# Optimization experiments

Hardware: AMD Instinct MI355X
Metric: run time of the kernel (lower is better)

Reference implementation:

```python
import jax, jax.numpy as jnp
import numpy as np

T, N, E, F_IN, H_GNN, H_OUT, RH, G, C = 8, 10000, 160000, 128, 128, 128, 128, 32, 10


def gcn_layer(x, src, dst, W, b):
    # PyG GCNConv: h = D^-1/2 (A+I) D^-1/2 (x W) + b, self-loops added, edge weight 1
    h = x @ W  # [N, H]
    ones = jnp.ones((E,), h.dtype)
    deg = jax.ops.segment_sum(ones, dst, num_segments=N) + 1.0  # +1 for self-loop
    dinv = jax.lax.rsqrt(deg)
    coef = dinv[src] * dinv[dst]  # [E]
    agg = jax.ops.segment_sum(h[src] * coef[:, None], dst, num_segments=N)
    agg = agg + h * (dinv * dinv)[:, None]  # self-loop term
    return agg + b


def snapshot_encode(x, edge_index, batch, W1, b1, W2, b2):
    src, dst = edge_index[0], edge_index[1]
    h = jax.nn.relu(gcn_layer(x, src, dst, W1, b1))
    h = jax.nn.relu(gcn_layer(h, src, dst, W2, b2))
    sums = jax.ops.segment_sum(h, batch, num_segments=G)  # global_mean_pool
    cnts = jax.ops.segment_sum(jnp.ones((N,), h.dtype), batch, num_segments=G)
    return sums / jnp.maximum(cnts, 1.0)[:, None]  # [G, H_OUT]


def gru_layer(seq, Wih, Whh, bih, bhh):
    # seq: [T, G, in]; torch nn.GRU cell equations
    H = Whh.shape[1]

    def step(h, xt):
        gi = xt @ Wih.T + bih
        gh = h @ Whh.T + bhh
        ir, iz, inn = jnp.split(gi, 3, axis=-1)
        hr, hz, hn = jnp.split(gh, 3, axis=-1)
        r = jax.nn.sigmoid(ir + hr)
        z = jax.nn.sigmoid(iz + hz)
        n = jnp.tanh(inn + r * hn)
        h_new = (1.0 - z) * n + z * h
        return h_new, h_new

    h0 = jnp.zeros((seq.shape[1], H), seq.dtype)
    hT, outs = jax.lax.scan(step, h0, seq)
    return outs, hT


def setup_inputs() -> dict:
    key = jax.random.key(0)
    ks = jax.random.split(key, 20)
    s = 0.05
    inp = {
        "x": jax.random.normal(ks[0], (T, N, F_IN), jnp.float32),
        "edge_index": jax.random.randint(ks[1], (T, 2, E), 0, N),
        "batch": jax.random.randint(ks[2], (T, N), 0, G),
        "W1": jax.random.normal(ks[3], (F_IN, H_GNN), jnp.float32) * s,
        "b1": jnp.zeros((H_GNN,), jnp.float32),
        "W2": jax.random.normal(ks[4], (H_GNN, H_OUT), jnp.float32) * s,
        "b2": jnp.zeros((H_OUT,), jnp.float32),
        "Wih0": jax.random.normal(ks[5], (3 * RH, H_OUT), jnp.float32) * s,
        "Whh0": jax.random.normal(ks[6], (3 * RH, RH), jnp.float32) * s,
        "bih0": jnp.zeros((3 * RH,), jnp.float32),
        "bhh0": jnp.zeros((3 * RH,), jnp.float32),
        "Wih1": jax.random.normal(ks[7], (3 * RH, RH), jnp.float32) * s,
        "Whh1": jax.random.normal(ks[8], (3 * RH, RH), jnp.float32) * s,
        "bih1": jnp.zeros((3 * RH,), jnp.float32),
        "bhh1": jnp.zeros((3 * RH,), jnp.float32),
        "Wc": jax.random.normal(ks[9], (C, RH), jnp.float32) * s,
        "bc": jnp.zeros((C,), jnp.float32),
    }
    return inp


def reference(x, edge_index, batch, W1, b1, W2, b2, Wih0, Whh0, bih0, bhh0,
              Wih1, Whh1, bih1, bhh1, Wc, bc):
    # per-snapshot GNN encode, vmapped over T snapshots -> [T, G, H_OUT]
    emb = jax.vmap(snapshot_encode, in_axes=(0, 0, 0, None, None, None, None))(
        x, edge_index, batch, W1, b1, W2, b2)
    outs, _ = gru_layer(emb, Wih0, Whh0, bih0, bhh0)
    _, hT = gru_layer(outs, Wih1, Whh1, bih1, bhh1)  # h_n[-1]: last layer final state
    return hT @ Wc.T + bc  # [G, C]
```

## Files before the change

### kernel.cpp

```cpp
#include <hip/hip_runtime.h>

#define T_ 8
#define N_ 10000
#define E_ 160000
#define G_ 32
#define C_ 10
#define F_ 128

typedef _Float16 f16;
typedef _Float16 f16x2 __attribute__((ext_vector_type(2)));
typedef _Float16 f16x4 __attribute__((ext_vector_type(4)));
typedef _Float16 f16x8 __attribute__((ext_vector_type(8)));
typedef float floatx4 __attribute__((ext_vector_type(4)));

static constexpr size_t ROWS = (size_t)T_ * N_;
static constexpr int SLICE = E_ / 8;

static constexpr size_t OFF_XH    = 0;
static constexpr size_t OFF_A1    = 20480000;
static constexpr size_t OFF_H1    = 40960000;
static constexpr size_t OFF_REC   = 61440000;
static constexpr size_t OFF_CNT   = 66560000;
static constexpr size_t OFF_DINV  = 69120000;
static constexpr size_t OFF_RP    = 69440000;
static constexpr size_t OFF_CNTG  = 69760032;
static constexpr size_t OFF_BRP   = 69761056;
static constexpr size_t OFF_WP    = 69762112;
static constexpr size_t OFF_BLIST = 69827648;
static constexpr size_t OFF_EMBH  = 70147648;
static constexpr size_t OFF_GPACK = 70213184;
static constexpr size_t OFF_GI0   = 70606400;
static constexpr size_t OFF_PART  = 70999616;

__device__ __forceinline__ float sig_fast(float x) {
  return __builtin_amdgcn_rcpf(1.0f + __builtin_amdgcn_exp2f(-1.4426950408889634f * x));
}
__device__ __forceinline__ float tanh_fast(float x) {
  return 1.0f - 2.0f * __builtin_amdgcn_rcpf(1.0f + __builtin_amdgcn_exp2f(2.8853900817779268f * x));
}

__global__ __launch_bounds__(1024) void hist_kernel(const int* __restrict__ ei,
                                                    const int* __restrict__ batch,
                                                    int* __restrict__ cnt,
                                                    int* __restrict__ cntG) {
  __shared__ int hL[N_];
  __shared__ int cL[G_];
  int b = blockIdx.x, tid = threadIdx.x;
  int t = b & 7, s = b >> 3;
  for (int i = tid; i < N_; i += 1024) hL[i] = 0;
  if (tid < G_) cL[tid] = 0;
  __syncthreads();
  const int* dstp = ei + (size_t)t * 2 * E_ + E_ + s * SLICE;
  for (int e4 = tid; e4 < SLICE / 4; e4 += 1024) {
    int4 d = *(const int4*)(dstp + e4 * 4);
    atomicAdd(&hL[d.x], 1); atomicAdd(&hL[d.y], 1);
    atomicAdd(&hL[d.z], 1); atomicAdd(&hL[d.w], 1);
  }
  if (s == 0)
    for (int n = tid; n < N_; n += 1024) atomicAdd(&cL[batch[t * N_ + n]], 1);
  __syncthreads();
  int* cp = cnt + ((size_t)t * 8 + s) * N_;
  for (int i = tid; i < N_; i += 1024) cp[i] = hL[i];
  if (s == 0 && tid < G_) cntG[t * G_ + tid] = cL[tid];
}

__global__ __launch_bounds__(1024) void scan_kernel(int* __restrict__ cnt,
                                                    int* __restrict__ rp,
                                                    float* __restrict__ dinv,
                                                    const int* __restrict__ cntG,
                                                    int* __restrict__ brp) {
  __shared__ int wsum[16];
  __shared__ int carry;
  int t = blockIdx.x, tid = threadIdx.x, lane = tid & 63, wid = tid >> 6;
  if (t == 8) {
    int v = (tid < 256) ? cntG[tid] : 0;
    for (int ofs = 1; ofs < 64; ofs <<= 1) {
      int u = __shfl_up(v, ofs);
      if (lane >= ofs) v += u;
    }
    if (lane == 63 && wid < 4) wsum[wid] = v;
    __syncthreads();
    if (tid < 256) {
      int base = 0;
      for (int w = 0; w < wid; ++w) base += wsum[w];
      if (tid == 0) brp[0] = 0;
      brp[tid + 1] = v + base;
    }
    return;
  }
  if (tid == 0) { carry = 0; rp[t * (N_ + 1)] = 0; }
  __syncthreads();
  for (int c0 = 0; c0 < N_; c0 += 1024) {
    int n = c0 + tid;
    int vs[8];
    int deg = 0;
    if (n < N_) {
#pragma unroll
      for (int s = 0; s < 8; ++s) {
        vs[s] = cnt[((size_t)t * 8 + s) * N_ + n];
        deg += vs[s];
      }
      dinv[t * N_ + n] = rsqrtf((float)deg + 1.0f);
    }
    int v = (n < N_) ? deg : 0;
    int v0 = v;
    for (int ofs = 1; ofs < 64; ofs <<= 1) {
      int u = __shfl_up(v, ofs);
      if (lane >= ofs) v += u;
    }
    if (lane == 63) wsum[wid] = v;
    __syncthreads();
    if (wid == 0) {
      int w = (lane < 16) ? wsum[lane] : 0;
      for (int ofs = 1; ofs < 16; ofs <<= 1) {
        int u = __shfl_up(w, ofs);
        if (lane >= ofs) w += u;
      }
      if (lane < 16) wsum[lane] = w;
    }
    __syncthreads();
    int base = carry + (wid ? wsum[wid - 1] : 0);
    if (n < N_) {
      rp[t * (N_ + 1) + n + 1] = base + v;
      int run = base + v - v0;
#pragma unroll
      for (int s = 0; s < 8; ++s) {
        int vv = vs[s];
        cnt[((size_t)t * 8 + s) * N_ + n] = run;
        run += vv;
      }
    }
    __syncthreads();
    if (tid == 0) carry += wsum[15];
    __syncthreads();
  }
}

__global__ __launch_bounds__(1024) void fill_kernel(const int* __restrict__ ei,
                                                    const int* __restrict__ base,
                                                    int* __restrict__ rec,
                                                    const int* __restrict__ batch,
                                                    const int* __restrict__ brp,
                                                    int* __restrict__ blist) {
  __shared__ int offL[N_];
  __shared__ int cb[G_];
  int b = blockIdx.x, tid = threadIdx.x;
  int t = b & 7, s = b >> 3;
  const int* bp = base + ((size_t)t * 8 + s) * N_;
  for (int i = tid; i < N_; i += 1024) offL[i] = bp[i];
  if (s == 0 && tid < G_) cb[tid] = brp[t * G_ + tid];
  __syncthreads();
  const int* srcp = ei + (size_t)t * 2 * E_ + s * SLICE;
  const int* dstp = srcp + E_;
  int* rt = rec + (size_t)t * E_;
  for (int e4 = tid; e4 < SLICE / 4; e4 += 1024) {
    int4 sv = *(const int4*)(srcp + e4 * 4);
    int4 dv = *(const int4*)(dstp + e4 * 4);
    int p0 = atomicAdd(&offL[dv.x], 1);
    int p1 = atomicAdd(&offL[dv.y], 1);
    int p2 = atomicAdd(&offL[dv.z], 1);
    int p3 = atomicAdd(&offL[dv.w], 1);
    rt[p0] = sv.x; rt[p1] = sv.y; rt[p2] = sv.z; rt[p3] = sv.w;
  }
  if (s == 0) {
    for (int n = tid; n < N_; n += 1024) {
      int g = batch[t * N_ + n];
      int p = atomicAdd(&cb[g], 1);
      blist[p] = t * N_ + n;
    }
  }
}

__global__ void cvt_kernel(const float* __restrict__ x, const float* __restrict__ dinv,
                           f16* __restrict__ xh) {
  size_t i = ((size_t)blockIdx.x * 256 + threadIdx.x) * 4;
  float4 v = *(const float4*)(x + i);
  float d = dinv[i >> 7];
  f16x4 o; o.x = (f16)(v.x * d); o.y = (f16)(v.y * d);
  o.z = (f16)(v.z * d); o.w = (f16)(v.w * d);
  *(f16x4*)(xh + i) = o;
}

__global__ void agg_kernel(const f16* __restrict__ X, f16* __restrict__ A,
                           const int* __restrict__ rp, const int* __restrict__ rec,
                           const float* __restrict__ dinv) {
  int wave = threadIdx.x >> 6, lane = threadIdx.x & 63;
  int b = blockIdx.x;
  int t = b & 7, i = b >> 3;
  int n = i * 4 + wave;
  int row = t * N_ + n;
  float ds = dinv[row];
  f16x2 xv = *(const f16x2*)(X + (size_t)row * F_ + 2 * lane);
  float a00 = (float)xv.x, a01 = (float)xv.y;
  float a10 = 0.f, a11 = 0.f, a20 = 0.f, a21 = 0.f, a30 = 0.f, a31 = 0.f;
  int beg = rp[t * (N_ + 1) + n], end = rp[t * (N_ + 1) + n + 1];
  beg = __builtin_amdgcn_readfirstlane(beg);
  end = __builtin_amdgcn_readfirstlane(end);
  const int* rc = rec + (size_t)t * E_;
  const f16* Xt = X + (size_t)t * N_ * F_;
  int e = beg;
  int i0 = 0, i1 = 0, i2 = 0, i3 = 0;
  if (e + 3 < end) { i0 = rc[e]; i1 = rc[e + 1]; i2 = rc[e + 2]; i3 = rc[e + 3]; }
  for (; e + 7 < end; e += 4) {
    int n0 = rc[e + 4], n1 = rc[e + 5], n2 = rc[e + 6], n3 = rc[e + 7];
    f16x2 h0 = *(const f16x2*)(Xt + (size_t)i0 * F_ + 2 * lane);
    f16x2 h1 = *(const f16x2*)(Xt + (size_t)i1 * F_ + 2 * lane);
    f16x2 h2 = *(const f16x2*)(Xt + (size_t)i2 * F_ + 2 * lane);
    f16x2 h3 = *(const f16x2*)(Xt + (size_t)i3 * F_ + 2 * lane);
    a00 += (float)h0.x; a01 += (float)h0.y;
    a10 += (float)h1.x; a11 += (float)h1.y;
    a20 += (float)h2.x; a21 += (float)h2.y;
    a30 += (float)h3.x; a31 += (float)h3.y;
    i0 = n0; i1 = n1; i2 = n2; i3 = n3;
  }
  if (e + 3 < end) {
    f16x2 h0 = *(const f16x2*)(Xt + (size_t)i0 * F_ + 2 * lane);
    f16x2 h1 = *(const f16x2*)(Xt + (size_t)i1 * F_ + 2 * lane);
    f16x2 h2 = *(const f16x2*)(Xt + (size_t)i2 * F_ + 2 * lane);
    f16x2 h3 = *(const f16x2*)(Xt + (size_t)i3 * F_ + 2 * lane);
    a00 += (float)h0.x; a01 += (float)h0.y;
    a10 += (float)h1.x; a11 += (float)h1.y;
    a20 += (float)h2.x; a21 += (float)h2.y;
    a30 += (float)h3.x; a31 += (float)h3.y;
    e += 4;
  }
  for (; e < end; ++e) {
    int s = rc[e];
    f16x2 hv = *(const f16x2*)(Xt + (size_t)s * F_ + 2 * lane);
    a00 += (float)hv.x; a01 += (float)hv.y;
  }
  float r0 = ds * ((a00 + a10) + (a20 + a30));
  float r1 = ds * ((a01 + a11) + (a21 + a31));
  f16x2 o; o.x = (f16)r0; o.y = (f16)r1;
  *(f16x2*)(A + (size_t)row * F_ + 2 * lane) = o;
}

__global__ void packall_kernel(const float* __restrict__ W1, const float* __restrict__ W2,
                               f16* __restrict__ Wp,
                               const float* __restrict__ A0, const float* __restrict__ A1,
                               const float* __restrict__ A2, const float* __restrict__ A3,
                               f16* __restrict__ gp) {
  int idx = blockIdx.x * 256 + threadIdx.x;
  if (idx < 32768) {
    const float* W = (idx < 16384) ? W1 : W2;
    int l = idx & 16383;
    int j = l & 7, lane = (l >> 3) & 63, ct = (l >> 9) & 7, kc = (l >> 12) & 3;
    int k = kc * 32 + ((lane >> 4) & 3) * 8 + j;
    int n = ct * 16 + (lane & 15);
    Wp[idx] = (f16)W[k * 128 + n];
  } else {
    int gidx = idx - 32768;
    int mat = gidx / 49152, l = gidx - mat * 49152;
    int j = l & 7, lane = (l >> 3) & 63, kc = (l >> 9) & 3, nt = l >> 11;
    int k = kc * 32 + ((lane >> 4) & 3) * 8 + j;
    int u = nt * 16 + (lane & 15);
    const float* W = (mat == 0) ? A0 : (mat == 1) ? A1 : (mat == 2) ? A2 : A3;
    gp[gidx] = (f16)W[u * 128 + k];
  }
}

__global__ __launch_bounds__(256) void gemm_kernel(const f16* __restrict__ A,
                                                   const f16* __restrict__ Wp,
                                                   const float* __restrict__ bias,
                                                   const float* __restrict__ scale,
                                                   f16* __restrict__ O) {
  __shared__ f16x8 Bp[2048];
  const f16x8* Wv = (const f16x8*)Wp;
  for (int i = threadIdx.x; i < 2048; i += 256) Bp[i] = Wv[i];
  __syncthreads();
  int wave = threadIdx.x >> 6, lane = threadIdx.x & 63;
  int quad = lane >> 4, m = lane & 15;
  int rowbase = blockIdx.x * 64 + wave * 16;
  const f16x8* Arow = (const f16x8*)(A + (size_t)(rowbase + m) * F_);
  floatx4 acc[8];
#pragma unroll
  for (int ct = 0; ct < 8; ++ct) { floatx4 z = {0.f, 0.f, 0.f, 0.f}; acc[ct] = z; }
#pragma unroll
  for (int kc = 0; kc < 4; ++kc) {
    f16x8 a = Arow[kc * 4 + quad];
#pragma unroll
    for (int ct = 0; ct < 8; ++ct)
      acc[ct] = __builtin_amdgcn_mfma_f32_16x16x32_f16(a, Bp[(kc * 8 + ct) * 64 + lane],
                                                       acc[ct], 0, 0, 0);
  }
  float sv[4];
#pragma unroll
  for (int r = 0; r < 4; ++r)
    sv[r] = scale ? scale[rowbase + quad * 4 + r] : 1.0f;
#pragma unroll
  for (int ct = 0; ct < 8; ++ct) {
    int colc = ct * 16 + m;
    float bv = bias[colc];
#pragma unroll
    for (int r = 0; r < 4; ++r) {
      int row = rowbase + quad * 4 + r;
      float v = fmaxf(acc[ct][r] + bv, 0.0f) * sv[r];
      O[(size_t)row * F_ + colc] = (f16)v;
    }
  }
}

__global__ void pool1_kernel(const f16* __restrict__ H, const int* __restrict__ brp,
                             const int* __restrict__ blist, float* __restrict__ part) {
  int b = blockIdx.x;
  int wave = threadIdx.x >> 6, lane = threadIdx.x & 63;
  int idx = b >> 1;
  int s = (b & 1) * 4 + wave;
  int beg = brp[idx], end = brp[idx + 1];
  beg = __builtin_amdgcn_readfirstlane(beg);
  end = __builtin_amdgcn_readfirstlane(end);
  int len = end - beg;
  int lo = beg + (int)(((long long)len * s) >> 3);
  int hi = beg + (int)(((long long)len * (s + 1)) >> 3);
  float a00 = 0.f, a01 = 0.f, a10 = 0.f, a11 = 0.f;
  float a20 = 0.f, a21 = 0.f, a30 = 0.f, a31 = 0.f;
  int e = lo;
  for (; e + 3 < hi; e += 4) {
    int r0 = blist[e], r1 = blist[e + 1], r2 = blist[e + 2], r3 = blist[e + 3];
    f16x2 v0 = *(const f16x2*)(H + (size_t)r0 * F_ + 2 * lane);
    f16x2 v1 = *(const f16x2*)(H + (size_t)r1 * F_ + 2 * lane);
    f16x2 v2 = *(const f16x2*)(H + (size_t)r2 * F_ + 2 * lane);
    f16x2 v3 = *(const f16x2*)(H + (size_t)r3 * F_ + 2 * lane);
    a00 += (float)v0.x; a01 += (float)v0.y;
    a10 += (float)v1.x; a11 += (float)v1.y;
    a20 += (float)v2.x; a21 += (float)v2.y;
    a30 += (float)v3.x; a31 += (float)v3.y;
  }
  for (; e < hi; ++e) {
    int r = blist[e];
    f16x2 v = *(const f16x2*)(H + (size_t)r * F_ + 2 * lane);
    a00 += (float)v.x; a01 += (float)v.y;
  }
  float2 o;
  o.x = (a00 + a10) + (a20 + a30);
  o.y = (a01 + a11) + (a21 + a31);
  *(float2*)(part + ((size_t)idx * 8 + s) * F_ + 2 * lane) = o;
}

__global__ void pool2_kernel(const float* __restrict__ part, const int* __restrict__ brp,
                             f16* __restrict__ embh) {
  int idx = blockIdx.x * 2 + (threadIdx.x >> 7);
  int f = threadIdx.x & 127;
  float s = 0.f;
#pragma unroll
  for (int k = 0; k < 8; ++k) s += part[((size_t)idx * 8 + k) * F_ + f];
  int cnt = brp[idx + 1] - brp[idx];
  embh[(size_t)idx * F_ + f] = (f16)(s / fmaxf((float)cnt, 1.0f));
}

__global__ __launch_bounds__(256) void gi0_kernel(const f16* __restrict__ embh,
                                                  const f16* __restrict__ gp,
                                                  float* __restrict__ gi0) {
  int wave = threadIdx.x >> 6, lane = threadIdx.x & 63;
  int quad = lane >> 4, mm = lane & 15;
  int rowbase = blockIdx.x * 64 + wave * 16;
  const f16* Arow = embh + (size_t)(rowbase + mm) * 128;
  floatx4 acc[24];
#pragma unroll
  for (int nt = 0; nt < 24; ++nt) { floatx4 z = {0.f, 0.f, 0.f, 0.f}; acc[nt] = z; }
#pragma unroll
  for (int kc = 0; kc < 4; ++kc) {
    f16x8 a = *(const f16x8*)(Arow + kc * 32 + quad * 8);
#pragma unroll
    for (int nt = 0; nt < 24; ++nt) {
      f16x8 b = *(const f16x8*)(gp + (size_t)(((nt * 4 + kc) * 64 + lane)) * 8);
      acc[nt] = __builtin_amdgcn_mfma_f32_16x16x32_f16(a, b, acc[nt], 0, 0, 0);
    }
  }
#pragma unroll
  for (int nt = 0; nt < 24; ++nt)
#pragma unroll
    for (int r = 0; r < 4; ++r)
      gi0[(size_t)(rowbase + quad * 4 + r) * 384 + nt * 16 + mm] = acc[nt][r];
}

__global__ __launch_bounds__(256, 1) void gru_fused(
    const f16* __restrict__ gp, const float* __restrict__ gi0,
    const float* __restrict__ bih0, const float* __restrict__ bhh0,
    const float* __restrict__ bih1, const float* __restrict__ bhh1,
    const float* __restrict__ Wc, const float* __restrict__ bc,
    float* __restrict__ out) {
  __shared__ f16 hb0[16 * 136];
  __shared__ f16 hb1[16 * 136];
  __shared__ float ghb[2 * 384];
  __shared__ float gib[2 * 384];
  __shared__ float h1s[2 * 128];
  int tid = threadIdx.x, wave = tid >> 6, lane = tid & 63;
  int quad = lane >> 4, mm = lane & 15;
  int g2 = tid >> 7, f = tid & 127;
  int bid = blockIdx.x;

  f16x8 B0[24], B1[24];
#pragma unroll
  for (int i = 0; i < 6; ++i)
#pragma unroll
    for (int kc = 0; kc < 4; ++kc) {
      size_t off = (size_t)((((wave * 6 + i) * 4 + kc) * 64 + lane)) * 8;
      B0[i * 4 + kc] = *(const f16x8*)(gp + 1 * 49152 + off);
      B1[i * 4 + kc] = *(const f16x8*)(gp + 3 * 49152 + off);
    }
  float br0 = bih0[f] + bhh0[f];
  float bz0 = bih0[128 + f] + bhh0[128 + f];
  float bni0 = bih0[256 + f], bnh0 = bhh0[256 + f];
  float br1 = bih1[f] + bhh1[f];
  float bz1 = bih1[128 + f] + bhh1[128 + f];
  float bni1 = bih1[256 + f], bnh1 = bhh1[256 + f];

  for (int i = tid; i < 16 * 136; i += 256) { hb0[i] = (f16)0.f; hb1[i] = (f16)0.f; }
  float h0 = 0.f, h1 = 0.f;
  __syncthreads();

  const f16* wih1 = gp + 2 * 49152;
  for (int t = 0; t < T_; ++t) {
    f16x8 Bs[24];
#pragma unroll
    for (int i = 0; i < 6; ++i)
#pragma unroll
      for (int kc = 0; kc < 4; ++kc)
        Bs[i * 4 + kc] = *(const f16x8*)(wih1 +
            (size_t)((((wave * 6 + i) * 4 + kc) * 64 + lane)) * 8);
    const float* gi = gi0 + (size_t)(t * G_ + bid * 2 + g2) * 384;
    float gir = gi[f], giz = gi[128 + f], gin = gi[256 + f];

    floatx4 acc[6];
#pragma unroll
    for (int i = 0; i < 6; ++i) { floatx4 z = {0.f, 0.f, 0.f, 0.f}; acc[i] = z; }
#pragma unroll
    for (int kc = 0; kc < 4; ++kc) {
      f16x8 a = *(const f16x8*)(hb0 + mm * 136 + kc * 32 + quad * 8);
#pragma unroll
      for (int i = 0; i < 6; ++i)
        acc[i] = __builtin_amdgcn_mfma_f32_16x16x32_f16(a, B0[i * 4 + kc], acc[i], 0, 0, 0);
    }
    if (quad == 0) {
#pragma unroll
      for (int i = 0; i < 6; ++i) {
        ghb[0 * 384 + wave * 96 + i * 16 + mm] = acc[i][0];
        ghb[1 * 384 + wave * 96 + i * 16 + mm] = acc[i][1];
      }
    }
    __syncthreads();

    {
      float hr = ghb[g2 * 384 + f];
      float hz = ghb[g2 * 384 + 128 + f];
      float hn = ghb[g2 * 384 + 256 + f];
      float r = sig_fast(gir + hr + br0);
      float z = sig_fast(giz + hz + bz0);
      float nn = tanh_fast(gin + bni0 + r * (hn + bnh0));
      h0 = (1.0f - z) * nn + z * h0;
      hb0[g2 * 136 + f] = (f16)h0;
    }
    __syncthreads();

    floatx4 accx[6], acch[6];
#pragma unroll
    for (int i = 0; i < 6; ++i) {
      floatx4 z = {0.f, 0.f, 0.f, 0.f}; accx[i] = z; acch[i] = z;
    }
#pragma unroll
    for (int kc = 0; kc < 4; ++kc) {
      f16x8 ax = *(const f16x8*)(hb0 + mm * 136 + kc * 32 + quad * 8);
      f16x8 ah = *(const f16x8*)(hb1 + mm * 136 + kc * 32 + quad * 8);
#pragma unroll
      for (int i = 0; i < 6; ++i) {
        accx[i] = __builtin_amdgcn_mfma_f32_16x16x32_f16(ax, Bs[i * 4 + kc], accx[i], 0, 0, 0);
        acch[i] = __builtin_amdgcn_mfma_f32_16x16x32_f16(ah, B1[i * 4 + kc], acch[i], 0, 0, 0);
      }
    }
    if (quad == 0) {
#pragma unroll
      for (int i = 0; i < 6; ++i) {
        gib[0 * 384 + wave * 96 + i * 16 + mm] = accx[i][0];
        gib[1 * 384 + wave * 96 + i * 16 + mm] = accx[i][1];
        ghb[0 * 384 + wave * 96 + i * 16 + mm] = acch[i][0];
        ghb[1 * 384 + wave * 96 + i * 16 + mm] = acch[i][1];
      }
    }
    __syncthreads();

    {
      float i1r = gib[g2 * 384 + f];
      float i1z = gib[g2 * 384 + 128 + f];
      float i1n = gib[g2 * 384 + 256 + f];
      float hr = ghb[g2 * 384 + f];
      float hz = ghb[g2 * 384 + 128 + f];
      float hn = ghb[g2 * 384 + 256 + f];
      float r = sig_fast(i1r + hr + br1);
      float z = sig_fast(i1z + hz + bz1);
      float nn = tanh_fast(i1n + bni1 + r * (hn + bnh1));
      h1 = (1.0f - z) * nn + z * h1;
      hb1[g2 * 136 + f] = (f16)h1;
    }
    __syncthreads();
  }

  h1s[g2 * 128 + f] = h1;
  __syncthreads();
  if (tid < 2 * C_) {
    int gg = tid / C_, c = tid - gg * C_;
    float s = bc[c];
    const float* wr = Wc + (size_t)c * 128;
    const float* hr = h1s + gg * 128;
    for (int k = 0; k < 128; k += 4) {
      float4 w = *(const float4*)(wr + k);
      s += hr[k] * w.x + hr[k + 1] * w.y + hr[k + 2] * w.z + hr[k + 3] * w.w;
    }
    out[(bid * 2 + gg) * C_ + c] = s;
  }
}

extern "C" void kernel_launch(void* const* d_in, const int* in_sizes, int n_in,
                              void* d_out, int out_size, void* d_ws, size_t ws_size,
                              hipStream_t stream) {
  const float* x    = (const float*)d_in[0];
  const int*   ei   = (const int*)d_in[1];
  const int*   batch= (const int*)d_in[2];
  const float* W1   = (const float*)d_in[3];
  const float* b1   = (const float*)d_in[4];
  const float* W2   = (const float*)d_in[5];
  const float* b2   = (const float*)d_in[6];
  const float* Wih0 = (const float*)d_in[7];
  const float* Whh0 = (const float*)d_in[8];
  const float* bih0 = (const float*)d_in[9];
  const float* bhh0 = (const float*)d_in[10];
  const float* Wih1 = (const float*)d_in[11];
  const float* Whh1 = (const float*)d_in[12];
  const float* bih1 = (const float*)d_in[13];
  const float* bhh1 = (const float*)d_in[14];
  const float* Wc   = (const float*)d_in[15];
  const float* bc   = (const float*)d_in[16];
  float* out = (float*)d_out;

  char* ws = (char*)d_ws;
  f16*   Xh    = (f16*)(ws + OFF_XH);
  f16*   A1    = (f16*)(ws + OFF_A1);
  f16*   H1    = (f16*)(ws + OFF_H1);
  f16*   A2    = A1;
  f16*   H2    = Xh;
  int*   rec   = (int*)(ws + OFF_REC);
  int*   cnt   = (int*)(ws + OFF_CNT);
  float* dinv  = (float*)(ws + OFF_DINV);
  int*   rp    = (int*)(ws + OFF_RP);
  int*   cntG  = (int*)(ws + OFF_CNTG);
  int*   brp   = (int*)(ws + OFF_BRP);
  f16*   Wp    = (f16*)(ws + OFF_WP);
  int*   blist = (int*)(ws + OFF_BLIST);
  f16*   embh  = (f16*)(ws + OFF_EMBH);
  f16*   gp    = (f16*)(ws + OFF_GPACK);
  float* gi0   = (float*)(ws + OFF_GI0);
  float* part  = (float*)(ws + OFF_PART);

  packall_kernel<<<896, 256, 0, stream>>>(W1, W2, Wp, Wih0, Whh0, Wih1, Whh1, gp);
  hist_kernel<<<64, 1024, 0, stream>>>(ei, batch, cnt, cntG);
  scan_kernel<<<9, 1024, 0, stream>>>(cnt, rp, dinv, cntG, brp);
  cvt_kernel<<<10000, 256, 0, stream>>>(x, dinv, Xh);
  fill_kernel<<<64, 1024, 0, stream>>>(ei, cnt, rec, batch, brp, blist);

  agg_kernel<<<20000, 256, 0, stream>>>(Xh, A1, rp, rec, dinv);
  gemm_kernel<<<1250, 256, 0, stream>>>(A1, Wp, b1, dinv, H1);
  agg_kernel<<<20000, 256, 0, stream>>>(H1, A2, rp, rec, dinv);
  gemm_kernel<<<1250, 256, 0, stream>>>(A2, Wp + 16384, b2, (const float*)nullptr, H2);

  pool1_kernel<<<512, 256, 0, stream>>>(H2, brp, blist, part);
  pool2_kernel<<<128, 256, 0, stream>>>(part, brp, embh);
  gi0_kernel<<<4, 256, 0, stream>>>(embh, gp, gi0);
  gru_fused<<<16, 256, 0, stream>>>(gp, gi0, bih0, bhh0, bih1, bhh1, Wc, bc, out);
}
```

Measured before the change: 307.9 us.

## Fuse neighbor aggregation into GEMM and fold pooling/gi0 into GRU kernel

Each GCN layer now runs as one kernel: a block gathers and sums neighbor rows for 64 nodes into shared memory, then multiplies that tile with the weight via MFMA. This removes the intermediate aggregate buffer round-trip and two launches. The final mean-pool reduction and the layer-0 input projection are moved into the GRU kernel's prologue, which removes two more small launches. The cost is less parallelism: 1256 blocks each doing 16 serial gathers per wave instead of 20000 blocks, so latency hiding during the gather may suffer.

Result: slower. 344.0 us (+11.7%).

```diff
diff --git a/kernel.cpp b/kernel.cpp
--- a/kernel.cpp
+++ b/kernel.cpp
@@ -27,9 +27,7 @@
 static constexpr size_t OFF_BRP   = 69761056;
 static constexpr size_t OFF_WP    = 69762112;
 static constexpr size_t OFF_BLIST = 69827648;
-static constexpr size_t OFF_EMBH  = 70147648;
 static constexpr size_t OFF_GPACK = 70213184;
-static constexpr size_t OFF_GI0   = 70606400;
 static constexpr size_t OFF_PART  = 70999616;
 
 __device__ __forceinline__ float sig_fast(float x) {
@@ -179,60 +177,6 @@
   f16x4 o; o.x = (f16)(v.x * d); o.y = (f16)(v.y * d);
   o.z = (f16)(v.z * d); o.w = (f16)(v.w * d);
   *(f16x4*)(xh + i) = o;
-}
-
-__global__ void agg_kernel(const f16* __restrict__ X, f16* __restrict__ A,
-                           const int* __restrict__ rp, const int* __restrict__ rec,
-                           const float* __restrict__ dinv) {
-  int wave = threadIdx.x >> 6, lane = threadIdx.x & 63;
-  int b = blockIdx.x;
-  int t = b & 7, i = b >> 3;
-  int n = i * 4 + wave;
-  int row = t * N_ + n;
-  float ds = dinv[row];
-  f16x2 xv = *(const f16x2*)(X + (size_t)row * F_ + 2 * lane);
-  float a00 = (float)xv.x, a01 = (float)xv.y;
-  float a10 = 0.f, a11 = 0.f, a20 = 0.f, a21 = 0.f, a30 = 0.f, a31 = 0.f;
-  int beg = rp[t * (N_ + 1) + n], end = rp[t * (N_ + 1) + n + 1];
-  beg = __builtin_amdgcn_readfirstlane(beg);
-  end = __builtin_amdgcn_readfirstlane(end);
-  const int* rc = rec + (size_t)t * E_;
-  const f16* Xt = X + (size_t)t * N_ * F_;
-  int e = beg;
-  int i0 = 0, i1 = 0, i2 = 0, i3 = 0;
-  if (e + 3 < end) { i0 = rc[e]; i1 = rc[e + 1]; i2 = rc[e + 2]; i3 = rc[e + 3]; }
-  for (; e + 7 < end; e += 4) {
-    int n0 = rc[e + 4], n1 = rc[e + 5], n2 = rc[e + 6], n3 = rc[e + 7];
-    f16x2 h0 = *(const f16x2*)(Xt + (size_t)i0 * F_ + 2 * lane);
-    f16x2 h1 = *(const f16x2*)(Xt + (size_t)i1 * F_ + 2 * lane);
-    f16x2 h2 = *(const f16x2*)(Xt + (size_t)i2 * F_ + 2 * lane);
-    f16x2 h3 = *(const f16x2*)(Xt + (size_t)i3 * F_ + 2 * lane);
-    a00 += (float)h0.x; a01 += (float)h0.y;
-    a10 += (float)h1.x; a11 += (float)h1.y;
-    a20 += (float)h2.x; a21 += (float)h2.y;
-    a30 += (float)h3.x; a31 += (float)h3.y;
-    i0 = n0; i1 = n1; i2 = n2; i3 = n3;
-  }
-  if (e + 3 < end) {
-    f16x2 h0 = *(const f16x2*)(Xt + (size_t)i0 * F_ + 2 * lane);
-    f16x2 h1 = *(const f16x2*)(Xt + (size_t)i1 * F_ + 2 * lane);
-    f16x2 h2 = *(const f16x2*)(Xt + (size_t)i2 * F_ + 2 * lane);
-    f16x2 h3 = *(const f16x2*)(Xt + (size_t)i3 * F_ + 2 * lane);
-    a00 += (float)h0.x; a01 += (float)h0.y;
-    a10 += (float)h1.x; a11 += (float)h1.y;
-    a20 += (float)h2.x; a21 += (float)h2.y;
-    a30 += (float)h3.x; a31 += (float)h3.y;
-    e += 4;
-  }
-  for (; e < end; ++e) {
-    int s = rc[e];
-    f16x2 hv = *(const f16x2*)(Xt + (size_t)s * F_ + 2 * lane);
-    a00 += (float)hv.x; a01 += (float)hv.y;
-  }
-  float r0 = ds * ((a00 + a10) + (a20 + a30));
-  float r1 = ds * ((a01 + a11) + (a21 + a31));
-  f16x2 o; o.x = (f16)r0; o.y = (f16)r1;
-  *(f16x2*)(A + (size_t)row * F_ + 2 * lane) = o;
 }
 
 __global__ void packall_kernel(const float* __restrict__ W1, const float* __restrict__ W2,
@@ -259,25 +203,90 @@
   }
 }
 
-__global__ __launch_bounds__(256) void gemm_kernel(const f16* __restrict__ A,
-                                                   const f16* __restrict__ Wp,
-                                                   const float* __restrict__ bias,
-                                                   const float* __restrict__ scale,
-                                                   f16* __restrict__ O) {
+template <int SCALE>
+__global__ __launch_bounds__(256) void agg_gemm_kernel(
+    const f16* __restrict__ X, const f16* __restrict__ Wp,
+    const float* __restrict__ bias, const float* __restrict__ dinv,
+    const int* __restrict__ rp, const int* __restrict__ rec,
+    f16* __restrict__ O) {
   __shared__ f16x8 Bp[2048];
+  __shared__ f16 At[64][136];
+  int tid = threadIdx.x;
   const f16x8* Wv = (const f16x8*)Wp;
-  for (int i = threadIdx.x; i < 2048; i += 256) Bp[i] = Wv[i];
-  __syncthreads();
-  int wave = threadIdx.x >> 6, lane = threadIdx.x & 63;
-  int quad = lane >> 4, m = lane & 15;
-  int rowbase = blockIdx.x * 64 + wave * 16;
-  const f16x8* Arow = (const f16x8*)(A + (size_t)(rowbase + m) * F_);
+  for (int i = tid; i < 2048; i += 256) Bp[i] = Wv[i];
+  __syncthreads();
+
+  int wave = tid >> 6, lane = tid & 63;
+  int b = blockIdx.x;
+  int t = b & 7, chunk = b >> 3;
+  int nbase = chunk * 64 + wave * 16;
+
+  const int* rpt = rp + t * (N_ + 1);
+  int rpv = 0;
+  if (lane <= 16 && nbase + lane <= N_) rpv = rpt[nbase + lane];
+  float dv = 0.f;
+  if (lane < 16 && nbase + lane < N_) dv = dinv[t * N_ + nbase + lane];
+
+  const f16* Xt = X + (size_t)t * N_ * F_;
+  const int* rc = rec + (size_t)t * E_;
+
+  for (int rr = 0; rr < 16; ++rr) {
+    int n = nbase + rr;
+    f16x2 o;
+    if (n < N_) {
+      int beg = __builtin_amdgcn_readfirstlane(__shfl(rpv, rr));
+      int end = __builtin_amdgcn_readfirstlane(__shfl(rpv, rr + 1));
+      float ds = __shfl(dv, rr);
+      f16x2 xv = *(const f16x2*)(Xt + (size_t)n * F_ + 2 * lane);
+      float a00 = (float)xv.x, a01 = (float)xv.y;
+      float a10 = 0.f, a11 = 0.f, a20 = 0.f, a21 = 0.f, a30 = 0.f, a31 = 0.f;
+      int e = beg;
+      int i0 = 0, i1 = 0, i2 = 0, i3 = 0;
+      if (e + 3 < end) { i0 = rc[e]; i1 = rc[e + 1]; i2 = rc[e + 2]; i3 = rc[e + 3]; }
+      for (; e + 7 < end; e += 4) {
+        int n0 = rc[e + 4], n1 = rc[e + 5], n2 = rc[e + 6], n3 = rc[e + 7];
+        f16x2 h0 = *(const f16x2*)(Xt + (size_t)i0 * F_ + 2 * lane);
+        f16x2 h1 = *(const f16x2*)(Xt + (size_t)i1 * F_ + 2 * lane);
+        f16x2 h2 = *(const f16x2*)(Xt + (size_t)i2 * F_ + 2 * lane);
+        f16x2 h3 = *(const f16x2*)(Xt + (size_t)i3 * F_ + 2 * lane);
+        a00 += (float)h0.x; a01 += (float)h0.y;
+        a10 += (float)h1.x; a11 += (float)h1.y;
+        a20 += (float)h2.x; a21 += (float)h2.y;
+        a30 += (float)h3.x; a31 += (float)h3.y;
+        i0 = n0; i1 = n1; i2 = n2; i3 = n3;
+      }
+      if (e + 3 < end) {
+        f16x2 h0 = *(const f16x2*)(Xt + (size_t)i0 * F_ + 2 * lane);
+        f16x2 h1 = *(const f16x2*)(Xt + (size_t)i1 * F_ + 2 * lane);
+        f16x2 h2 = *(const f16x2*)(Xt + (size_t)i2 * F_ + 2 * lane);
+        f16x2 h3 = *(const f16x2*)(Xt + (size_t)i3 * F_ + 2 * lane);
+        a00 += (float)h0.x; a01 += (float)h0.y;
+        a10 += (float)h1.x; a11 += (float)h1.y;
+        a20 += (float)h2.x; a21 += (float)h2.y;
+        a30 += (float)h3.x; a31 += (float)h3.y;
+        e += 4;
+      }
+      for (; e < end; ++e) {
+        int s = rc[e];
+        f16x2 hv = *(const f16x2*)(Xt + (size_t)s * F_ + 2 * lane);
+        a00 += (float)hv.x; a01 += (float)hv.y;
+      }
+      float r0 = ds * ((a00 + a10) + (a20 + a30));
+      float r1 = ds * ((a01 + a11) + (a21 + a31));
+      o.x = (f16)r0; o.y = (f16)r1;
+    } else {
+      o.x = (f16)0.f; o.y = (f16)0.f;
+    }
+    *(f16x2*)(&At[wave * 16 + rr][2 * lane]) = o;
+  }
+
+  int quad = lane >> 4, mm = lane & 15;
   floatx4 acc[8];
 #pragma unroll
   for (int ct = 0; ct < 8; ++ct) { floatx4 z = {0.f, 0.f, 0.f, 0.f}; acc[ct] = z; }
 #pragma unroll
   for (int kc = 0; kc < 4; ++kc) {
-    f16x8 a = Arow[kc * 4 + quad];
+    f16x8 a = *(const f16x8*)(&At[wave * 16 + mm][kc * 32 + quad * 8]);
 #pragma unroll
     for (int ct = 0; ct < 8; ++ct)
       acc[ct] = __builtin_amdgcn_mfma_f32_16x16x32_f16(a, Bp[(kc * 8 + ct) * 64 + lane],
@@ -286,16 +295,18 @@
   float sv[4];
 #pragma unroll
   for (int r = 0; r < 4; ++r)
-    sv[r] = scale ? scale[rowbase + quad * 4 + r] : 1.0f;
+    sv[r] = SCALE ? __shfl(dv, quad * 4 + r) : 1.0f;
 #pragma unroll
   for (int ct = 0; ct < 8; ++ct) {
-    int colc = ct * 16 + m;
+    int colc = ct * 16 + mm;
     float bv = bias[colc];
 #pragma unroll
     for (int r = 0; r < 4; ++r) {
-      int row = rowbase + quad * 4 + r;
-      float v = fmaxf(acc[ct][r] + bv, 0.0f) * sv[r];
-      O[(size_t)row * F_ + colc] = (f16)v;
+      int n = nbase + quad * 4 + r;
+      if (n < N_) {
+        float v = fmaxf(acc[ct][r] + bv, 0.0f) * sv[r];
+        O[((size_t)t * N_ + n) * F_ + colc] = (f16)v;
+      }
     }
   }
 }
@@ -337,49 +348,15 @@
   *(float2*)(part + ((size_t)idx * 8 + s) * F_ + 2 * lane) = o;
 }
 
-__global__ void pool2_kernel(const float* __restrict__ part, const int* __restrict__ brp,
-                             f16* __restrict__ embh) {
-  int idx = blockIdx.x * 2 + (threadIdx.x >> 7);
-  int f = threadIdx.x & 127;
-  float s = 0.f;
-#pragma unroll
-  for (int k = 0; k < 8; ++k) s += part[((size_t)idx * 8 + k) * F_ + f];
-  int cnt = brp[idx + 1] - brp[idx];
-  embh[(size_t)idx * F_ + f] = (f16)(s / fmaxf((float)cnt, 1.0f));
-}
-
-__global__ __launch_bounds__(256) void gi0_kernel(const f16* __restrict__ embh,
-                                                  const f16* __restrict__ gp,
-                                                  float* __restrict__ gi0) {
-  int wave = threadIdx.x >> 6, lane = threadIdx.x & 63;
-  int quad = lane >> 4, mm = lane & 15;
-  int rowbase = blockIdx.x * 64 + wave * 16;
-  const f16* Arow = embh + (size_t)(rowbase + mm) * 128;
-  floatx4 acc[24];
-#pragma unroll
-  for (int nt = 0; nt < 24; ++nt) { floatx4 z = {0.f, 0.f, 0.f, 0.f}; acc[nt] = z; }
-#pragma unroll
-  for (int kc = 0; kc < 4; ++kc) {
-    f16x8 a = *(const f16x8*)(Arow + kc * 32 + quad * 8);
-#pragma unroll
-    for (int nt = 0; nt < 24; ++nt) {
-      f16x8 b = *(const f16x8*)(gp + (size_t)(((nt * 4 + kc) * 64 + lane)) * 8);
-      acc[nt] = __builtin_amdgcn_mfma_f32_16x16x32_f16(a, b, acc[nt], 0, 0, 0);
-    }
-  }
-#pragma unroll
-  for (int nt = 0; nt < 24; ++nt)
-#pragma unroll
-    for (int r = 0; r < 4; ++r)
-      gi0[(size_t)(rowbase + quad * 4 + r) * 384 + nt * 16 + mm] = acc[nt][r];
-}
-
-__global__ __launch_bounds__(256, 1) void gru_fused(
-    const f16* __restrict__ gp, const float* __restrict__ gi0,
+__global__ __launch_bounds__(256, 1) void gru_mega(
+    const f16* __restrict__ gp, const float* __restrict__ part,
+    const int* __restrict__ brp,
     const float* __restrict__ bih0, const float* __restrict__ bhh0,
     const float* __restrict__ bih1, const float* __restrict__ bhh1,
     const float* __restrict__ Wc, const float* __restrict__ bc,
     float* __restrict__ out) {
+  __shared__ f16 emb_l[16][136];
+  __shared__ float gib0[16][384];
   __shared__ f16 hb0[16 * 136];
   __shared__ f16 hb1[16 * 136];
   __shared__ float ghb[2 * 384];
@@ -390,6 +367,48 @@
   int g2 = tid >> 7, f = tid & 127;
   int bid = blockIdx.x;
 
+  {
+    int r = tid >> 4;
+    int fb = (tid & 15) * 8;
+    int idx = (r >> 1) * G_ + bid * 2 + (r & 1);
+    float s[8] = {0.f, 0.f, 0.f, 0.f, 0.f, 0.f, 0.f, 0.f};
+#pragma unroll
+    for (int k = 0; k < 8; ++k) {
+      const float* p = part + ((size_t)idx * 8 + k) * F_ + fb;
+      float4 v0 = *(const float4*)p;
+      float4 v1 = *(const float4*)(p + 4);
+      s[0] += v0.x; s[1] += v0.y; s[2] += v0.z; s[3] += v0.w;
+      s[4] += v1.x; s[5] += v1.y; s[6] += v1.z; s[7] += v1.w;
+    }
+    float d = fmaxf((float)(brp[idx + 1] - brp[idx]), 1.0f);
+    f16x8 ev;
+#pragma unroll
+    for (int j = 0; j < 8; ++j) ev[j] = (f16)(s[j] / d);
+    *(f16x8*)(&emb_l[r][fb]) = ev;
+  }
+  __syncthreads();
+
+  {
+    floatx4 acc[6];
+#pragma unroll
+    for (int i = 0; i < 6; ++i) { floatx4 z = {0.f, 0.f, 0.f, 0.f}; acc[i] = z; }
+#pragma unroll
+    for (int kc = 0; kc < 4; ++kc) {
+      f16x8 a = *(const f16x8*)(&emb_l[mm][kc * 32 + quad * 8]);
+#pragma unroll
+      for (int i = 0; i < 6; ++i) {
+        int nt = wave * 6 + i;
+        f16x8 bf = *(const f16x8*)(gp + (size_t)((nt * 4 + kc) * 64 + lane) * 8);
+        acc[i] = __builtin_amdgcn_mfma_f32_16x16x32_f16(a, bf, acc[i], 0, 0, 0);
+      }
+    }
+#pragma unroll
+    for (int i = 0; i < 6; ++i)
+#pragma unroll
+      for (int r = 0; r < 4; ++r)
+        gib0[quad * 4 + r][(wave * 6 + i) * 16 + mm] = acc[i][r];
+  }
+
   f16x8 B0[24], B1[24];
 #pragma unroll
   for (int i = 0; i < 6; ++i)
@@ -419,7 +438,7 @@
       for (int kc = 0; kc < 4; ++kc)
         Bs[i * 4 + kc] = *(const f16x8*)(wih1 +
             (size_t)((((wave * 6 + i) * 4 + kc) * 64 + lane)) * 8);
-    const float* gi = gi0 + (size_t)(t * G_ + bid * 2 + g2) * 384;
+    const float* gi = &gib0[t * 2 + g2][0];
     float gir = gi[f], giz = gi[128 + f], gin = gi[256 + f];
 
     floatx4 acc[6];
@@ -534,9 +553,7 @@
 
   char* ws = (char*)d_ws;
   f16*   Xh    = (f16*)(ws + OFF_XH);
-  f16*   A1    = (f16*)(ws + OFF_A1);
   f16*   H1    = (f16*)(ws + OFF_H1);
-  f16*   A2    = A1;
   f16*   H2    = Xh;
   int*   rec   = (int*)(ws + OFF_REC);
   int*   cnt   = (int*)(ws + OFF_CNT);
@@ -546,9 +563,7 @@
   int*   brp   = (int*)(ws + OFF_BRP);
   f16*   Wp    = (f16*)(ws + OFF_WP);
   int*   blist = (int*)(ws + OFF_BLIST);
-  f16*   embh  = (f16*)(ws + OFF_EMBH);
   f16*   gp    = (f16*)(ws + OFF_GPACK);
-  float* gi0   = (float*)(ws + OFF_GI0);
   float* part  = (float*)(ws + OFF_PART);
 
   packall_kernel<<<896, 256, 0, stream>>>(W1, W2, Wp, Wih0, Whh0, Wih1, Whh1, gp);
@@ -557,13 +572,9 @@
   cvt_kernel<<<10000, 256, 0, stream>>>(x, dinv, Xh);
   fill_kernel<<<64, 1024, 0, stream>>>(ei, cnt, rec, batch, brp, blist);
 
-  agg_kernel<<<20000, 256, 0, stream>>>(Xh, A1, rp, rec, dinv);
-  gemm_kernel<<<1250, 256, 0, stream>>>(A1, Wp, b1, dinv, H1);
-  agg_kernel<<<20000, 256, 0, stream>>>(H1, A2, rp, rec, dinv);
-  gemm_kernel<<<1250, 256, 0, stream>>>(A2, Wp + 16384, b2, (const float*)nullptr, H2);
+  agg_gemm_kernel<1><<<8 * 157, 256, 0, stream>>>(Xh, Wp, b1, dinv, rp, rec, H1);
+  agg_gemm_kernel<0><<<8 * 157, 256, 0, stream>>>(H1, Wp + 16384, b2, dinv, rp, rec, H2);
 
   pool1_kernel<<<512, 256, 0, stream>>>(H2, brp, blist, part);
-  pool2_kernel<<<128, 256, 0, stream>>>(part, brp, embh);
-  gi0_kernel<<<4, 256, 0, stream>>>(embh, gp, gi0);
-  gru_fused<<<16, 256, 0, stream>>>(gp, gi0, bih0, bhh0, bih1, bhh1, Wc, bc, out);
-}
+  gru_mega<<<16, 256, 0, stream>>>(gp, part, brp, bih0, bhh0, bih1, bhh1, Wc, bc, out);
+}
```
